# Performance work log

Hardware: AMD Instinct MI355X
Metric: run time of the kernel (lower is better)

## Reference

```python
import jax, jax.numpy as jnp
import numpy as np

HIDDEN = 128
GRID = 8
NEIGH = 4.0
CELL = NEIGH / GRID


def setup_inputs() -> dict:
    key = jax.random.key(0)
    k1, k2, k3, k4 = jax.random.split(key, 4)
    B, N = 64, 64
    hidden_states = jax.random.normal(k1, (B, N, HIDDEN), dtype=jnp.float32)
    positions = jax.random.normal(k2, (B, N, 2), dtype=jnp.float32)
    fan_in = HIDDEN * GRID * GRID
    bound = 1.0 / np.sqrt(fan_in)
    W = jax.random.uniform(k3, (HIDDEN, fan_in), minval=-bound, maxval=bound, dtype=jnp.float32)
    b = jax.random.uniform(k4, (HIDDEN,), minval=-bound, maxval=bound, dtype=jnp.float32)
    return {"hidden_states": hidden_states, "positions": positions, "W": W, "b": b}


def reference(hidden_states, positions, W, b):
    B, N, H = hidden_states.shape
    G, G2 = GRID, GRID * GRID
    # rel[b, i, j] = positions[b, j] - positions[b, i]  (offset of neighbor j in agent i's frame)
    rel = positions[:, None, :, :] - positions[:, :, None, :]  # [B, N, N, 2]
    # torch .long() truncates toward zero; jnp astype(int32) does the same, and after
    # clamping to [0, G-1] this matches the original exactly.
    gx = ((rel[..., 0] + NEIGH / 2) / CELL).astype(jnp.int32).clip(0, G - 1)
    gy = ((rel[..., 1] + NEIGH / 2) / CELL).astype(jnp.int32).clip(0, G - 1)
    cell = gx * G + gy  # [B, N(i), N(j)] flat grid-cell index (gx-major, matching view order)
    # Exclude self (j == i) from pooling.
    not_self = (1.0 - jnp.eye(N, dtype=hidden_states.dtype))  # [N(i), N(j)]
    onehot = jax.nn.one_hot(cell, G2, dtype=hidden_states.dtype) * not_self[None, :, :, None]
    # Scatter-add neighbor hidden states into each agent's grid: [B, N(i), G2, H]
    grid = jnp.einsum('bijc,bjh->bich', onehot, hidden_states)
    grid_flat = grid.reshape(B, N, G2 * H)  # (gx, gy, h) flatten order == torch .view
    pooled = grid_flat @ W.T + b  # [B, N, H]
    return pooled
```

## Files before the change

### kernel.cpp

```cpp
#include <hip/hip_runtime.h>
#include <hip/hip_bf16.h>
#include <stdint.h>


typedef __attribute__((ext_vector_type(8))) short bf16x8;
typedef __attribute__((ext_vector_type(4))) float f32x4;

#define NCHUNK 8
#define CPB 8

__device__ inline unsigned short bf16bits(float x) {
    __hip_bfloat16 h = __float2bfloat16(x);
    return *reinterpret_cast<unsigned short*>(&h);
}

__global__ __launch_bounds__(512)
void gp_wconv(const float* __restrict__ W, __hip_bfloat16* __restrict__ Wb)
{
    __shared__ __attribute__((aligned(16))) __hip_bfloat16 Wl[128][136];
    const int c = blockIdx.x, t = threadIdx.x;
    #pragma unroll
    for (int q = 0; q < 8; ++q) {
        int flat = q * 512 + t;
        int ho = flat >> 5, k4 = flat & 31;
        float4 v = *(const float4*)(W + (size_t)ho * 8192 + c * 128 + k4 * 4);
        __hip_bfloat16* d = &Wl[ho][k4 * 4];
        d[0] = __float2bfloat16(v.x); d[1] = __float2bfloat16(v.y);
        d[2] = __float2bfloat16(v.z); d[3] = __float2bfloat16(v.w);
    }
    __syncthreads();
    #pragma unroll
    for (int q = 0; q < 4; ++q) {
        int flat = q * 512 + t;
        int hg = flat >> 7, ho = flat & 127;
        bf16x8 v = *(const bf16x8*)&Wl[ho][hg * 8];
        *(bf16x8*)(Wb + (size_t)c * 16384 + (size_t)flat * 8) = v;
    }
}

__global__ __launch_bounds__(512, 4)
void gp_main(const float* __restrict__ hid, const float* __restrict__ pos,
             const __hip_bfloat16* __restrict__ Wb, float* __restrict__ partial)
{
    __shared__ __attribute__((aligned(16))) __hip_bfloat16 Hs[16 * 64 * 8];
    __shared__ __attribute__((aligned(16))) __hip_bfloat16 Zt[2][8 * 128 * 8];
    __shared__ __attribute__((aligned(16))) __hip_bfloat16 Ms[2][8 * 64 * 8];
    __shared__ unsigned char cellt[64 * 64];
    __shared__ float ps[128];

    const int t = threadIdx.x;
    const int b = blockIdx.x & 63, chunk = blockIdx.x >> 6;
    const int w = t >> 6, lane = t & 63;
    const int l15 = lane & 15, kg = lane >> 4;
    const int mw = w & 1, nw = w >> 1;

    if (t < 128) ps[t] = pos[(size_t)b * 128 + t];
    __syncthreads();

    #pragma unroll
    for (int q = 0; q < 8; ++q) {
        int idx = q * 512 + t;
        int i = idx >> 6, j = idx & 63;
        float rx = ps[j * 2 + 0] - ps[i * 2 + 0];
        float ry = ps[j * 2 + 1] - ps[i * 2 + 1];
        int gx = (int)((rx + 2.0f) * 2.0f);
        int gy = (int)((ry + 2.0f) * 2.0f);
        gx = gx < 0 ? 0 : (gx > 7 ? 7 : gx);
        gy = gy < 0 ? 0 : (gy > 7 ? 7 : gy);
        cellt[idx] = (i == j) ? 255 : (unsigned char)(gx * 8 + gy);
    }
    #pragma unroll
    for (int q = 0; q < 2; ++q) {
        int idx = q * 512 + t;
        int hg = idx >> 6, j = idx & 63;
        const float* src = hid + ((size_t)b * 64 + j) * 128 + hg * 8;
        float4 v0 = *(const float4*)src;
        float4 v1 = *(const float4*)(src + 4);
        __hip_bfloat16* d = &Hs[(hg * 64 + j) * 8];
        d[0] = __float2bfloat16(v0.x); d[1] = __float2bfloat16(v0.y);
        d[2] = __float2bfloat16(v0.z); d[3] = __float2bfloat16(v0.w);
        d[4] = __float2bfloat16(v1.x); d[5] = __float2bfloat16(v1.y);
        d[6] = __float2bfloat16(v1.z); d[7] = __float2bfloat16(v1.w);
    }
    __syncthreads();

    bf16x8 afr[2][4];
    #pragma unroll
    for (int ks = 0; ks < 4; ++ks) {
        int hg = ks * 4 + kg;
        afr[0][ks] = *(const bf16x8*)&Hs[(hg * 64 + mw * 32 + l15) * 8];
        afr[1][ks] = *(const bf16x8*)&Hs[(hg * 64 + mw * 32 + 16 + l15) * 8];
    }

    f32x4 acc[2][2];
    #pragma unroll
    for (int fm = 0; fm < 2; ++fm)
        #pragma unroll
        for (int fn = 0; fn < 2; ++fn)
            acc[fm][fn] = (f32x4){0.f, 0.f, 0.f, 0.f};

    #pragma unroll 2
    for (int cc = 0; cc < CPB; ++cc) {
        const int p = cc & 1;
        const int c = chunk * CPB + cc;

        const __hip_bfloat16* wc = Wb + (size_t)c * 16384;
        bf16x8 bfr[4][2];
        #pragma unroll
        for (int ks = 0; ks < 4; ++ks) {
            int hg = ks * 4 + kg;
            bfr[ks][0] = *(const bf16x8*)(wc + ((size_t)hg * 128 + nw * 32 + l15) * 8);
            bfr[ks][1] = *(const bf16x8*)(wc + ((size_t)hg * 128 + nw * 32 + 16 + l15) * 8);
        }

        {
            int i = t & 63, jg = t >> 6;
            const unsigned char* cr = &cellt[i * 64 + jg * 8];
            __hip_bfloat16* d = &Ms[p][(jg * 64 + i) * 8];
            #pragma unroll
            for (int e = 0; e < 8; ++e)
                d[e] = __float2bfloat16(cr[e] == c ? 1.0f : 0.0f);
        }

        f32x4 z[2][2];
        #pragma unroll
        for (int fm = 0; fm < 2; ++fm)
            #pragma unroll
            for (int fn = 0; fn < 2; ++fn)
                z[fm][fn] = (f32x4){0.f, 0.f, 0.f, 0.f};
        #pragma unroll
        for (int ks = 0; ks < 4; ++ks) {
            z[0][0] = __builtin_amdgcn_mfma_f32_16x16x32_bf16(afr[0][ks], bfr[ks][0], z[0][0], 0, 0, 0);
            z[0][1] = __builtin_amdgcn_mfma_f32_16x16x32_bf16(afr[0][ks], bfr[ks][1], z[0][1], 0, 0, 0);
            z[1][0] = __builtin_amdgcn_mfma_f32_16x16x32_bf16(afr[1][ks], bfr[ks][0], z[1][0], 0, 0, 0);
            z[1][1] = __builtin_amdgcn_mfma_f32_16x16x32_bf16(afr[1][ks], bfr[ks][1], z[1][1], 0, 0, 0);
        }

        #pragma unroll
        for (int fm = 0; fm < 2; ++fm) {
            #pragma unroll
            for (int fn = 0; fn < 2; ++fn) {
                int j0 = mw * 32 + fm * 16 + kg * 4;
                int jg = j0 >> 3, e0 = j0 & 7;
                int ho = nw * 32 + fn * 16 + l15;
                union { unsigned short us[4]; uint2 v; } pk;
                pk.us[0] = bf16bits(z[fm][fn][0]);
                pk.us[1] = bf16bits(z[fm][fn][1]);
                pk.us[2] = bf16bits(z[fm][fn][2]);
                pk.us[3] = bf16bits(z[fm][fn][3]);
                *(uint2*)((char*)&Zt[p][0] + ((size_t)(jg * 128 + ho) * 8 + e0) * 2) = pk.v;
            }
        }
        __syncthreads();

        #pragma unroll
        for (int ks = 0; ks < 2; ++ks) {
            int jg = ks * 4 + kg;
            bf16x8 a0 = *(const bf16x8*)&Ms[p][(jg * 64 + mw * 32 + l15) * 8];
            bf16x8 a1 = *(const bf16x8*)&Ms[p][(jg * 64 + mw * 32 + 16 + l15) * 8];
            bf16x8 b0 = *(const bf16x8*)&Zt[p][(jg * 128 + nw * 32 + l15) * 8];
            bf16x8 b1 = *(const bf16x8*)&Zt[p][(jg * 128 + nw * 32 + 16 + l15) * 8];
            acc[0][0] = __builtin_amdgcn_mfma_f32_16x16x32_bf16(a0, b0, acc[0][0], 0, 0, 0);
            acc[0][1] = __builtin_amdgcn_mfma_f32_16x16x32_bf16(a0, b1, acc[0][1], 0, 0, 0);
            acc[1][0] = __builtin_amdgcn_mfma_f32_16x16x32_bf16(a1, b0, acc[1][0], 0, 0, 0);
            acc[1][1] = __builtin_amdgcn_mfma_f32_16x16x32_bf16(a1, b1, acc[1][1], 0, 0, 0);
        }
    }

    float* pb = partial + (((size_t)chunk * 64 + b) * 64) * 128;
    #pragma unroll
    for (int fm = 0; fm < 2; ++fm)
        #pragma unroll
        for (int fn = 0; fn < 2; ++fn)
            #pragma unroll
            for (int r = 0; r < 4; ++r) {
                int i = mw * 32 + fm * 16 + kg * 4 + r;
                int ho = nw * 32 + fn * 16 + l15;
                pb[(size_t)i * 128 + ho] = acc[fm][fn][r];
            }
}

__global__ __launch_bounds__(512)
void gp_reduce(const float* __restrict__ partial, const float* __restrict__ bias,
               float* __restrict__ out)
{
    int gid = blockIdx.x * 512 + threadIdx.x;
    int ho4 = gid & 31;
    float4 a = *(const float4*)(bias + ho4 * 4);
    #pragma unroll
    for (int ch = 0; ch < NCHUNK; ++ch) {
        float4 v = *(const float4*)(partial + (size_t)ch * 524288 + (size_t)gid * 4);
        a.x += v.x; a.y += v.y; a.z += v.z; a.w += v.w;
    }
    *(float4*)(out + (size_t)gid * 4) = a;
}

extern "C" void kernel_launch(void* const* d_in, const int* in_sizes, int n_in,
                              void* d_out, int out_size, void* d_ws, size_t ws_size,
                              hipStream_t stream)
{
    const float* hid  = (const float*)d_in[0];
    const float* pos  = (const float*)d_in[1];
    const float* W    = (const float*)d_in[2];
    const float* bias = (const float*)d_in[3];
    float* out = (float*)d_out;

    __hip_bfloat16* Wb = (__hip_bfloat16*)d_ws;
    float* partial = (float*)((char*)d_ws + (size_t)2097152);

    hipLaunchKernelGGL(gp_wconv,  dim3(64),          dim3(512), 0, stream, W, Wb);
    hipLaunchKernelGGL(gp_main,   dim3(NCHUNK * 64), dim3(512), 0, stream, hid, pos, Wb, partial);
    hipLaunchKernelGGL(gp_reduce, dim3(256),         dim3(512), 0, stream, partial, bias, out);
}
```

Baseline: 34.25 us.

## Replace dense one-hot MFMA scatter with sparse per-cell neighbor lists

The second-stage dense MFMA against a mostly-zero one-hot mask is replaced. The kernel now builds per-agent, per-cell neighbor index lists in shared memory and sums the matching Z rows with scalar bf16-to-fp32 adds. Z is stored in an XOR-swizzled layout to reduce bank conflicts, and the accumulation for each cell is deferred one iteration so it overlaps the next cell's MFMA. W fragments are prefetched one cell ahead. The cost is data-dependent loop trip counts, which cause divergence and load imbalance across lanes, plus extra list-building passes over the cell table.

```diff
diff --git a/kernel.cpp b/kernel.cpp
--- a/kernel.cpp
+++ b/kernel.cpp
@@ -12,6 +12,11 @@
 __device__ inline unsigned short bf16bits(float x) {
     __hip_bfloat16 h = __float2bfloat16(x);
     return *reinterpret_cast<unsigned short*>(&h);
+}
+__device__ inline float bf2f(short u) {
+    union { unsigned int i; float f; } v;
+    v.i = ((unsigned int)(unsigned short)u) << 16;
+    return v.f;
 }
 
 __global__ __launch_bounds__(512)
@@ -43,16 +48,18 @@
              const __hip_bfloat16* __restrict__ Wb, float* __restrict__ partial)
 {
     __shared__ __attribute__((aligned(16))) __hip_bfloat16 Hs[16 * 64 * 8];
-    __shared__ __attribute__((aligned(16))) __hip_bfloat16 Zt[2][8 * 128 * 8];
-    __shared__ __attribute__((aligned(16))) __hip_bfloat16 Ms[2][8 * 64 * 8];
+    __shared__ __attribute__((aligned(16))) __hip_bfloat16 Zt[2][64 * 128];
     __shared__ unsigned char cellt[64 * 64];
+    __shared__ unsigned char listj[64 * 64];
+    __shared__ unsigned char cnt8[64][8];
+    __shared__ unsigned char offs[64][9];
     __shared__ float ps[128];
 
     const int t = threadIdx.x;
     const int b = blockIdx.x & 63, chunk = blockIdx.x >> 6;
     const int w = t >> 6, lane = t & 63;
     const int l15 = lane & 15, kg = lane >> 4;
-    const int mw = w & 1, nw = w >> 1;
+    const int wm = w & 3, wn = w >> 2;
 
     if (t < 128) ps[t] = pos[(size_t)b * 128 + t];
     __syncthreads();
@@ -84,100 +91,142 @@
     }
     __syncthreads();
 
-    bf16x8 afr[2][4];
+    bf16x8 hf[2][4];
     #pragma unroll
     for (int ks = 0; ks < 4; ++ks) {
         int hg = ks * 4 + kg;
-        afr[0][ks] = *(const bf16x8*)&Hs[(hg * 64 + mw * 32 + l15) * 8];
-        afr[1][ks] = *(const bf16x8*)&Hs[(hg * 64 + mw * 32 + 16 + l15) * 8];
-    }
-
-    f32x4 acc[2][2];
-    #pragma unroll
-    for (int fm = 0; fm < 2; ++fm)
-        #pragma unroll
-        for (int fn = 0; fn < 2; ++fn)
-            acc[fm][fn] = (f32x4){0.f, 0.f, 0.f, 0.f};
-
-    #pragma unroll 2
+        hf[0][ks] = *(const bf16x8*)&Hs[(hg * 64 + wn * 32 + l15) * 8];
+        hf[1][ks] = *(const bf16x8*)&Hs[(hg * 64 + wn * 32 + 16 + l15) * 8];
+    }
+
+    {
+        int i = t >> 3, c = t & 7;
+        int target = chunk * 8 + c;
+        int n = 0;
+        for (int j = 0; j < 64; ++j) n += (cellt[i * 64 + j] == target);
+        cnt8[i][c] = (unsigned char)n;
+    }
+    __syncthreads();
+    if (t < 64) {
+        int s = 0;
+        offs[t][0] = 0;
+        #pragma unroll
+        for (int c = 0; c < 8; ++c) { s += cnt8[t][c]; offs[t][c + 1] = (unsigned char)s; }
+    }
+    __syncthreads();
+    {
+        int i = t >> 3, c = t & 7;
+        int target = chunk * 8 + c;
+        int n = offs[i][c];
+        for (int j = 0; j < 64; ++j)
+            if (cellt[i * 64 + j] == target) listj[i * 64 + (n++)] = (unsigned char)j;
+    }
+
+    bf16x8 wf[2][4];
+    {
+        const __hip_bfloat16* wc = Wb + (size_t)(chunk * 8) * 16384;
+        #pragma unroll
+        for (int ks = 0; ks < 4; ++ks) {
+            int hg = ks * 4 + kg;
+            wf[0][ks] = *(const bf16x8*)(wc + ((size_t)hg * 128 + wm * 32 + l15) * 8);
+            wf[1][ks] = *(const bf16x8*)(wc + ((size_t)hg * 128 + wm * 32 + 16 + l15) * 8);
+        }
+    }
+
+    float acc[2][8];
+    #pragma unroll
+    for (int p4 = 0; p4 < 2; ++p4)
+        #pragma unroll
+        for (int e = 0; e < 8; ++e) acc[p4][e] = 0.f;
+
+    const int hog = lane & 15, ig = lane >> 4;
+    __syncthreads();
+
     for (int cc = 0; cc < CPB; ++cc) {
         const int p = cc & 1;
-        const int c = chunk * CPB + cc;
-
-        const __hip_bfloat16* wc = Wb + (size_t)c * 16384;
-        bf16x8 bfr[4][2];
+
+        if (cc > 0) {
+            const int cl = cc - 1;
+            #pragma unroll
+            for (int p4 = 0; p4 < 2; ++p4) {
+                int i = w * 8 + p4 * 4 + ig;
+                int n1 = offs[i][cl + 1];
+                for (int n = offs[i][cl]; n < n1; ++n) {
+                    int j = listj[i * 64 + n];
+                    int boff = (hog * 16) ^ ((j & 7) << 4);
+                    bf16x8 v = *(const bf16x8*)((const char*)&Zt[p ^ 1][0] + j * 256 + boff);
+                    #pragma unroll
+                    for (int e = 0; e < 8; ++e) acc[p4][e] += bf2f(v[e]);
+                }
+            }
+        }
+
+        f32x4 z[2][2];
+        #pragma unroll
+        for (int fm = 0; fm < 2; ++fm)
+            #pragma unroll
+            for (int fn = 0; fn < 2; ++fn) z[fm][fn] = (f32x4){0.f, 0.f, 0.f, 0.f};
         #pragma unroll
         for (int ks = 0; ks < 4; ++ks) {
-            int hg = ks * 4 + kg;
-            bfr[ks][0] = *(const bf16x8*)(wc + ((size_t)hg * 128 + nw * 32 + l15) * 8);
-            bfr[ks][1] = *(const bf16x8*)(wc + ((size_t)hg * 128 + nw * 32 + 16 + l15) * 8);
-        }
-
-        {
-            int i = t & 63, jg = t >> 6;
-            const unsigned char* cr = &cellt[i * 64 + jg * 8];
-            __hip_bfloat16* d = &Ms[p][(jg * 64 + i) * 8];
-            #pragma unroll
-            for (int e = 0; e < 8; ++e)
-                d[e] = __float2bfloat16(cr[e] == c ? 1.0f : 0.0f);
-        }
-
-        f32x4 z[2][2];
-        #pragma unroll
-        for (int fm = 0; fm < 2; ++fm)
-            #pragma unroll
-            for (int fn = 0; fn < 2; ++fn)
-                z[fm][fn] = (f32x4){0.f, 0.f, 0.f, 0.f};
-        #pragma unroll
-        for (int ks = 0; ks < 4; ++ks) {
-            z[0][0] = __builtin_amdgcn_mfma_f32_16x16x32_bf16(afr[0][ks], bfr[ks][0], z[0][0], 0, 0, 0);
-            z[0][1] = __builtin_amdgcn_mfma_f32_16x16x32_bf16(afr[0][ks], bfr[ks][1], z[0][1], 0, 0, 0);
-            z[1][0] = __builtin_amdgcn_mfma_f32_16x16x32_bf16(afr[1][ks], bfr[ks][0], z[1][0], 0, 0, 0);
-            z[1][1] = __builtin_amdgcn_mfma_f32_16x16x32_bf16(afr[1][ks], bfr[ks][1], z[1][1], 0, 0, 0);
+            z[0][0] = __builtin_amdgcn_mfma_f32_16x16x32_bf16(wf[0][ks], hf[0][ks], z[0][0], 0, 0, 0);
+            z[0][1] = __builtin_amdgcn_mfma_f32_16x16x32_bf16(wf[0][ks], hf[1][ks], z[0][1], 0, 0, 0);
+            z[1][0] = __builtin_amdgcn_mfma_f32_16x16x32_bf16(wf[1][ks], hf[0][ks], z[1][0], 0, 0, 0);
+            z[1][1] = __builtin_amdgcn_mfma_f32_16x16x32_bf16(wf[1][ks], hf[1][ks], z[1][1], 0, 0, 0);
         }
 
         #pragma unroll
         for (int fm = 0; fm < 2; ++fm) {
             #pragma unroll
             for (int fn = 0; fn < 2; ++fn) {
-                int j0 = mw * 32 + fm * 16 + kg * 4;
-                int jg = j0 >> 3, e0 = j0 & 7;
-                int ho = nw * 32 + fn * 16 + l15;
+                int j   = wn * 32 + fn * 16 + l15;
+                int ho0 = wm * 32 + fm * 16 + kg * 4;
+                int boff = (ho0 * 2) ^ ((j & 7) << 4);
                 union { unsigned short us[4]; uint2 v; } pk;
                 pk.us[0] = bf16bits(z[fm][fn][0]);
                 pk.us[1] = bf16bits(z[fm][fn][1]);
                 pk.us[2] = bf16bits(z[fm][fn][2]);
                 pk.us[3] = bf16bits(z[fm][fn][3]);
-                *(uint2*)((char*)&Zt[p][0] + ((size_t)(jg * 128 + ho) * 8 + e0) * 2) = pk.v;
+                *(uint2*)((char*)&Zt[p][0] + j * 256 + boff) = pk.v;
+            }
+        }
+
+        if (cc < CPB - 1) {
+            const __hip_bfloat16* wc = Wb + (size_t)(chunk * 8 + cc + 1) * 16384;
+            #pragma unroll
+            for (int ks = 0; ks < 4; ++ks) {
+                int hg = ks * 4 + kg;
+                wf[0][ks] = *(const bf16x8*)(wc + ((size_t)hg * 128 + wm * 32 + l15) * 8);
+                wf[1][ks] = *(const bf16x8*)(wc + ((size_t)hg * 128 + wm * 32 + 16 + l15) * 8);
             }
         }
         __syncthreads();
-
-        #pragma unroll
-        for (int ks = 0; ks < 2; ++ks) {
-            int jg = ks * 4 + kg;
-            bf16x8 a0 = *(const bf16x8*)&Ms[p][(jg * 64 + mw * 32 + l15) * 8];
-            bf16x8 a1 = *(const bf16x8*)&Ms[p][(jg * 64 + mw * 32 + 16 + l15) * 8];
-            bf16x8 b0 = *(const bf16x8*)&Zt[p][(jg * 128 + nw * 32 + l15) * 8];
-            bf16x8 b1 = *(const bf16x8*)&Zt[p][(jg * 128 + nw * 32 + 16 + l15) * 8];
-            acc[0][0] = __builtin_amdgcn_mfma_f32_16x16x32_bf16(a0, b0, acc[0][0], 0, 0, 0);
-            acc[0][1] = __builtin_amdgcn_mfma_f32_16x16x32_bf16(a0, b1, acc[0][1], 0, 0, 0);
-            acc[1][0] = __builtin_amdgcn_mfma_f32_16x16x32_bf16(a1, b0, acc[1][0], 0, 0, 0);
-            acc[1][1] = __builtin_amdgcn_mfma_f32_16x16x32_bf16(a1, b1, acc[1][1], 0, 0, 0);
+    }
+
+    {
+        const int cl = CPB - 1;
+        #pragma unroll
+        for (int p4 = 0; p4 < 2; ++p4) {
+            int i = w * 8 + p4 * 4 + ig;
+            int n1 = offs[i][cl + 1];
+            for (int n = offs[i][cl]; n < n1; ++n) {
+                int j = listj[i * 64 + n];
+                int boff = (hog * 16) ^ ((j & 7) << 4);
+                bf16x8 v = *(const bf16x8*)((const char*)&Zt[(CPB - 1) & 1][0] + j * 256 + boff);
+                #pragma unroll
+                for (int e = 0; e < 8; ++e) acc[p4][e] += bf2f(v[e]);
+            }
         }
     }
 
     float* pb = partial + (((size_t)chunk * 64 + b) * 64) * 128;
     #pragma unroll
-    for (int fm = 0; fm < 2; ++fm)
-        #pragma unroll
-        for (int fn = 0; fn < 2; ++fn)
-            #pragma unroll
-            for (int r = 0; r < 4; ++r) {
-                int i = mw * 32 + fm * 16 + kg * 4 + r;
-                int ho = nw * 32 + fn * 16 + l15;
-                pb[(size_t)i * 128 + ho] = acc[fm][fn][r];
-            }
+    for (int p4 = 0; p4 < 2; ++p4) {
+        int i = w * 8 + p4 * 4 + ig;
+        float4 v0 = make_float4(acc[p4][0], acc[p4][1], acc[p4][2], acc[p4][3]);
+        float4 v1 = make_float4(acc[p4][4], acc[p4][5], acc[p4][6], acc[p4][7]);
+        *(float4*)(pb + (size_t)i * 128 + hog * 8) = v0;
+        *(float4*)(pb + (size_t)i * 128 + hog * 8 + 4) = v1;
+    }
 }
 
 __global__ __launch_bounds__(512)
```

After: 47.71 us. 39.3% more time.

## Double-buffer W chunks in LDS via async global_load_lds prefetch

Applied to the files above, without the earlier changes.

Each per-cell W tile is no longer loaded from global memory into registers per wave. The block now copies it into a double-buffered LDS array with global_load_lds, prefetching the next cell's tile while the current one is computed, and the MFMA B-fragments are read from LDS. This aims to hide global load latency and remove the duplicate W loads across waves. In exchange, LDS use grows by 64KB and the occupancy hint drops from 4 to 2, which cuts resident blocks per CU. It also relies on the barrier correctly waiting for the asynchronous LDS loads.

```diff
diff --git a/kernel.cpp b/kernel.cpp
--- a/kernel.cpp
+++ b/kernel.cpp
@@ -8,6 +8,12 @@
 
 #define NCHUNK 8
 #define CPB 8
+
+__device__ inline void load_lds16(const void* g, void* l) {
+    __builtin_amdgcn_global_load_lds(
+        (const __attribute__((address_space(1))) unsigned int*)g,
+        (__attribute__((address_space(3))) unsigned int*)l, 16, 0, 0);
+}
 
 __device__ inline unsigned short bf16bits(float x) {
     __hip_bfloat16 h = __float2bfloat16(x);
@@ -38,10 +44,11 @@
     }
 }
 
-__global__ __launch_bounds__(512, 4)
+__global__ __launch_bounds__(512, 2)
 void gp_main(const float* __restrict__ hid, const float* __restrict__ pos,
              const __hip_bfloat16* __restrict__ Wb, float* __restrict__ partial)
 {
+    __shared__ __attribute__((aligned(16))) __hip_bfloat16 Ws[2][16 * 128 * 8];
     __shared__ __attribute__((aligned(16))) __hip_bfloat16 Hs[16 * 64 * 8];
     __shared__ __attribute__((aligned(16))) __hip_bfloat16 Zt[2][8 * 128 * 8];
     __shared__ __attribute__((aligned(16))) __hip_bfloat16 Ms[2][8 * 64 * 8];
@@ -82,6 +89,15 @@
         d[4] = __float2bfloat16(v1.x); d[5] = __float2bfloat16(v1.y);
         d[6] = __float2bfloat16(v1.z); d[7] = __float2bfloat16(v1.w);
     }
+
+    {
+        const char* gsrc = (const char*)(Wb + (size_t)(chunk * 8) * 16384);
+        #pragma unroll
+        for (int q = 0; q < 4; ++q) {
+            int off = q * 8192 + t * 16;
+            load_lds16(gsrc + off, (char*)&Ws[0][0] + off);
+        }
+    }
     __syncthreads();
 
     bf16x8 afr[2][4];
@@ -104,13 +120,13 @@
         const int p = cc & 1;
         const int c = chunk * CPB + cc;
 
-        const __hip_bfloat16* wc = Wb + (size_t)c * 16384;
-        bf16x8 bfr[4][2];
-        #pragma unroll
-        for (int ks = 0; ks < 4; ++ks) {
-            int hg = ks * 4 + kg;
-            bfr[ks][0] = *(const bf16x8*)(wc + ((size_t)hg * 128 + nw * 32 + l15) * 8);
-            bfr[ks][1] = *(const bf16x8*)(wc + ((size_t)hg * 128 + nw * 32 + 16 + l15) * 8);
+        if (cc < CPB - 1) {
+            const char* gsrc = (const char*)(Wb + (size_t)(c + 1) * 16384);
+            #pragma unroll
+            for (int q = 0; q < 4; ++q) {
+                int off = q * 8192 + t * 16;
+                load_lds16(gsrc + off, (char*)&Ws[p ^ 1][0] + off);
+            }
         }
 
         {
@@ -126,14 +142,16 @@
         #pragma unroll
         for (int fm = 0; fm < 2; ++fm)
             #pragma unroll
-            for (int fn = 0; fn < 2; ++fn)
-                z[fm][fn] = (f32x4){0.f, 0.f, 0.f, 0.f};
+            for (int fn = 0; fn < 2; ++fn) z[fm][fn] = (f32x4){0.f, 0.f, 0.f, 0.f};
         #pragma unroll
         for (int ks = 0; ks < 4; ++ks) {
-            z[0][0] = __builtin_amdgcn_mfma_f32_16x16x32_bf16(afr[0][ks], bfr[ks][0], z[0][0], 0, 0, 0);
-            z[0][1] = __builtin_amdgcn_mfma_f32_16x16x32_bf16(afr[0][ks], bfr[ks][1], z[0][1], 0, 0, 0);
-            z[1][0] = __builtin_amdgcn_mfma_f32_16x16x32_bf16(afr[1][ks], bfr[ks][0], z[1][0], 0, 0, 0);
-            z[1][1] = __builtin_amdgcn_mfma_f32_16x16x32_bf16(afr[1][ks], bfr[ks][1], z[1][1], 0, 0, 0);
+            int hg = ks * 4 + kg;
+            bf16x8 b0 = *(const bf16x8*)&Ws[p][(hg * 128 + nw * 32 + l15) * 8];
+            bf16x8 b1 = *(const bf16x8*)&Ws[p][(hg * 128 + nw * 32 + 16 + l15) * 8];
+            z[0][0] = __builtin_amdgcn_mfma_f32_16x16x32_bf16(afr[0][ks], b0, z[0][0], 0, 0, 0);
+            z[0][1] = __builtin_amdgcn_mfma_f32_16x16x32_bf16(afr[0][ks], b1, z[0][1], 0, 0, 0);
+            z[1][0] = __builtin_amdgcn_mfma_f32_16x16x32_bf16(afr[1][ks], b0, z[1][0], 0, 0, 0);
+            z[1][1] = __builtin_amdgcn_mfma_f32_16x16x32_bf16(afr[1][ks], b1, z[1][1], 0, 0, 0);
         }
 
         #pragma unroll
```

Measured after the change: 37.93 us. +10.7%, slower.

## Restructure gp_main into per-wave independent pipelines without block barriers

Applied to the files above, without the earlier changes.

Halves the block to 256 threads, with each wave owning a 32-column output slice and all 64 rows. Each wave now computes its own Z tile into a private swizzled LDS scratch and reads it back, so the per-cell __syncthreads is gone. The one-hot mask is built in registers from preloaded cell bytes instead of staged through LDS. W fragments for the next cell are double-buffered in registers. The cost is higher register pressure (a 4x4 array of A fragments, 8 accumulators and two W buffers) and fewer waves per block, which may reduce occupancy.

```diff
diff --git a/kernel.cpp b/kernel.cpp
--- a/kernel.cpp
+++ b/kernel.cpp
@@ -5,6 +5,7 @@
 
 typedef __attribute__((ext_vector_type(8))) short bf16x8;
 typedef __attribute__((ext_vector_type(4))) float f32x4;
+typedef unsigned int u32;
 
 #define NCHUNK 8
 #define CPB 8
@@ -38,13 +39,12 @@
     }
 }
 
-__global__ __launch_bounds__(512, 4)
+__global__ __launch_bounds__(256, 2)
 void gp_main(const float* __restrict__ hid, const float* __restrict__ pos,
              const __hip_bfloat16* __restrict__ Wb, float* __restrict__ partial)
 {
     __shared__ __attribute__((aligned(16))) __hip_bfloat16 Hs[16 * 64 * 8];
-    __shared__ __attribute__((aligned(16))) __hip_bfloat16 Zt[2][8 * 128 * 8];
-    __shared__ __attribute__((aligned(16))) __hip_bfloat16 Ms[2][8 * 64 * 8];
+    __shared__ u32 zscr[4][1024];
     __shared__ unsigned char cellt[64 * 64];
     __shared__ float ps[128];
 
@@ -52,14 +52,13 @@
     const int b = blockIdx.x & 63, chunk = blockIdx.x >> 6;
     const int w = t >> 6, lane = t & 63;
     const int l15 = lane & 15, kg = lane >> 4;
-    const int mw = w & 1, nw = w >> 1;
 
     if (t < 128) ps[t] = pos[(size_t)b * 128 + t];
     __syncthreads();
 
     #pragma unroll
-    for (int q = 0; q < 8; ++q) {
-        int idx = q * 512 + t;
+    for (int q = 0; q < 16; ++q) {
+        int idx = q * 256 + t;
         int i = idx >> 6, j = idx & 63;
         float rx = ps[j * 2 + 0] - ps[i * 2 + 0];
         float ry = ps[j * 2 + 1] - ps[i * 2 + 1];
@@ -70,8 +69,8 @@
         cellt[idx] = (i == j) ? 255 : (unsigned char)(gx * 8 + gy);
     }
     #pragma unroll
-    for (int q = 0; q < 2; ++q) {
-        int idx = q * 512 + t;
+    for (int q = 0; q < 4; ++q) {
+        int idx = q * 256 + t;
         int hg = idx >> 6, j = idx & 63;
         const float* src = hid + ((size_t)b * 64 + j) * 128 + hg * 8;
         float4 v0 = *(const float4*)src;
@@ -84,99 +83,125 @@
     }
     __syncthreads();
 
-    bf16x8 afr[2][4];
-    #pragma unroll
-    for (int ks = 0; ks < 4; ++ks) {
-        int hg = ks * 4 + kg;
-        afr[0][ks] = *(const bf16x8*)&Hs[(hg * 64 + mw * 32 + l15) * 8];
-        afr[1][ks] = *(const bf16x8*)&Hs[(hg * 64 + mw * 32 + 16 + l15) * 8];
-    }
-
-    f32x4 acc[2][2];
-    #pragma unroll
-    for (int fm = 0; fm < 2; ++fm)
-        #pragma unroll
-        for (int fn = 0; fn < 2; ++fn)
-            acc[fm][fn] = (f32x4){0.f, 0.f, 0.f, 0.f};
-
-    #pragma unroll 2
+    bf16x8 a[4][4];
+    #pragma unroll
+    for (int jt = 0; jt < 4; ++jt)
+        #pragma unroll
+        for (int ks = 0; ks < 4; ++ks) {
+            int hg = ks * 4 + kg;
+            a[jt][ks] = *(const bf16x8*)&Hs[(hg * 64 + jt * 16 + l15) * 8];
+        }
+    uint2 cs[4][2];
+    #pragma unroll
+    for (int mt = 0; mt < 4; ++mt)
+        #pragma unroll
+        for (int ks2 = 0; ks2 < 2; ++ks2)
+            cs[mt][ks2] = *(const uint2*)&cellt[(mt * 16 + l15) * 64 + ks2 * 32 + kg * 8];
+
+    f32x4 acc[4][2];
+    #pragma unroll
+    for (int mt = 0; mt < 4; ++mt) {
+        acc[mt][0] = (f32x4){0.f, 0.f, 0.f, 0.f};
+        acc[mt][1] = (f32x4){0.f, 0.f, 0.f, 0.f};
+    }
+
+    u32* zw = &zscr[w][0];
+
+    bf16x8 wf[2][4][2];
+    {
+        const __hip_bfloat16* wc = Wb + (size_t)(chunk * CPB) * 16384;
+        #pragma unroll
+        for (int ks = 0; ks < 4; ++ks)
+            #pragma unroll
+            for (int fh = 0; fh < 2; ++fh)
+                wf[0][ks][fh] = *(const bf16x8*)(wc +
+                    ((size_t)(ks * 4 + kg) * 128 + w * 32 + fh * 16 + l15) * 8);
+    }
+
+    #pragma unroll
     for (int cc = 0; cc < CPB; ++cc) {
         const int p = cc & 1;
         const int c = chunk * CPB + cc;
 
-        const __hip_bfloat16* wc = Wb + (size_t)c * 16384;
-        bf16x8 bfr[4][2];
-        #pragma unroll
-        for (int ks = 0; ks < 4; ++ks) {
-            int hg = ks * 4 + kg;
-            bfr[ks][0] = *(const bf16x8*)(wc + ((size_t)hg * 128 + nw * 32 + l15) * 8);
-            bfr[ks][1] = *(const bf16x8*)(wc + ((size_t)hg * 128 + nw * 32 + 16 + l15) * 8);
-        }
-
-        {
-            int i = t & 63, jg = t >> 6;
-            const unsigned char* cr = &cellt[i * 64 + jg * 8];
-            __hip_bfloat16* d = &Ms[p][(jg * 64 + i) * 8];
-            #pragma unroll
-            for (int e = 0; e < 8; ++e)
-                d[e] = __float2bfloat16(cr[e] == c ? 1.0f : 0.0f);
-        }
-
-        f32x4 z[2][2];
-        #pragma unroll
-        for (int fm = 0; fm < 2; ++fm)
-            #pragma unroll
-            for (int fn = 0; fn < 2; ++fn)
-                z[fm][fn] = (f32x4){0.f, 0.f, 0.f, 0.f};
-        #pragma unroll
-        for (int ks = 0; ks < 4; ++ks) {
-            z[0][0] = __builtin_amdgcn_mfma_f32_16x16x32_bf16(afr[0][ks], bfr[ks][0], z[0][0], 0, 0, 0);
-            z[0][1] = __builtin_amdgcn_mfma_f32_16x16x32_bf16(afr[0][ks], bfr[ks][1], z[0][1], 0, 0, 0);
-            z[1][0] = __builtin_amdgcn_mfma_f32_16x16x32_bf16(afr[1][ks], bfr[ks][0], z[1][0], 0, 0, 0);
-            z[1][1] = __builtin_amdgcn_mfma_f32_16x16x32_bf16(afr[1][ks], bfr[ks][1], z[1][1], 0, 0, 0);
-        }
-
-        #pragma unroll
-        for (int fm = 0; fm < 2; ++fm) {
-            #pragma unroll
-            for (int fn = 0; fn < 2; ++fn) {
-                int j0 = mw * 32 + fm * 16 + kg * 4;
-                int jg = j0 >> 3, e0 = j0 & 7;
-                int ho = nw * 32 + fn * 16 + l15;
-                union { unsigned short us[4]; uint2 v; } pk;
-                pk.us[0] = bf16bits(z[fm][fn][0]);
-                pk.us[1] = bf16bits(z[fm][fn][1]);
-                pk.us[2] = bf16bits(z[fm][fn][2]);
-                pk.us[3] = bf16bits(z[fm][fn][3]);
-                *(uint2*)((char*)&Zt[p][0] + ((size_t)(jg * 128 + ho) * 8 + e0) * 2) = pk.v;
-            }
-        }
-        __syncthreads();
-
-        #pragma unroll
-        for (int ks = 0; ks < 2; ++ks) {
-            int jg = ks * 4 + kg;
-            bf16x8 a0 = *(const bf16x8*)&Ms[p][(jg * 64 + mw * 32 + l15) * 8];
-            bf16x8 a1 = *(const bf16x8*)&Ms[p][(jg * 64 + mw * 32 + 16 + l15) * 8];
-            bf16x8 b0 = *(const bf16x8*)&Zt[p][(jg * 128 + nw * 32 + l15) * 8];
-            bf16x8 b1 = *(const bf16x8*)&Zt[p][(jg * 128 + nw * 32 + 16 + l15) * 8];
-            acc[0][0] = __builtin_amdgcn_mfma_f32_16x16x32_bf16(a0, b0, acc[0][0], 0, 0, 0);
-            acc[0][1] = __builtin_amdgcn_mfma_f32_16x16x32_bf16(a0, b1, acc[0][1], 0, 0, 0);
-            acc[1][0] = __builtin_amdgcn_mfma_f32_16x16x32_bf16(a1, b0, acc[1][0], 0, 0, 0);
-            acc[1][1] = __builtin_amdgcn_mfma_f32_16x16x32_bf16(a1, b1, acc[1][1], 0, 0, 0);
+        if (cc + 1 < CPB) {
+            const __hip_bfloat16* wc = Wb + (size_t)(c + 1) * 16384;
+            #pragma unroll
+            for (int ks = 0; ks < 4; ++ks)
+                #pragma unroll
+                for (int fh = 0; fh < 2; ++fh)
+                    wf[p ^ 1][ks][fh] = *(const bf16x8*)(wc +
+                        ((size_t)(ks * 4 + kg) * 128 + w * 32 + fh * 16 + l15) * 8);
+        }
+
+        f32x4 z[4][2];
+        #pragma unroll
+        for (int jt = 0; jt < 4; ++jt) {
+            z[jt][0] = (f32x4){0.f, 0.f, 0.f, 0.f};
+            z[jt][1] = (f32x4){0.f, 0.f, 0.f, 0.f};
+        }
+        #pragma unroll
+        for (int ks = 0; ks < 4; ++ks)
+            #pragma unroll
+            for (int jt = 0; jt < 4; ++jt) {
+                z[jt][0] = __builtin_amdgcn_mfma_f32_16x16x32_bf16(a[jt][ks], wf[p][ks][0], z[jt][0], 0, 0, 0);
+                z[jt][1] = __builtin_amdgcn_mfma_f32_16x16x32_bf16(a[jt][ks], wf[p][ks][1], z[jt][1], 0, 0, 0);
+            }
+
+        #pragma unroll
+        for (int jt = 0; jt < 4; ++jt)
+            #pragma unroll
+            for (int fh = 0; fh < 2; ++fh) {
+                u32 p0 = (u32)bf16bits(z[jt][fh][0]) | ((u32)bf16bits(z[jt][fh][1]) << 16);
+                u32 p1 = (u32)bf16bits(z[jt][fh][2]) | ((u32)bf16bits(z[jt][fh][3]) << 16);
+                int X = ((jt * 2 + (kg >> 1)) & 3) << 3;
+                int a32 = (((jt * 8 + kg * 2) * 32) + fh * 16 + l15) ^ X;
+                zw[a32] = p0;
+                zw[a32 + 32] = p1;
+            }
+
+        bf16x8 b2[2][2];
+        #pragma unroll
+        for (int ks2 = 0; ks2 < 2; ++ks2)
+            #pragma unroll
+            for (int fh = 0; fh < 2; ++fh) {
+                int base = (((ks2 * 16 + kg * 4) * 32) + fh * 16 + l15) ^ (kg << 3);
+                union { u32 wd[4]; bf16x8 v; } r;
+                r.wd[0] = zw[base];
+                r.wd[1] = zw[base + 32];
+                r.wd[2] = zw[base + 64];
+                r.wd[3] = zw[base + 96];
+                b2[ks2][fh] = r.v;
+            }
+
+        #pragma unroll
+        for (int mt = 0; mt < 4; ++mt) {
+            #pragma unroll
+            for (int ks2 = 0; ks2 < 2; ++ks2) {
+                union { u32 wd[4]; bf16x8 v; } m;
+                u32 s0 = cs[mt][ks2].x, s1 = cs[mt][ks2].y;
+                #pragma unroll
+                for (int k = 0; k < 4; ++k) {
+                    u32 s = (k < 2) ? s0 : s1;
+                    u32 b0 = (s >> ((k & 1) * 16)) & 0xFFu;
+                    u32 b1 = (s >> ((k & 1) * 16 + 8)) & 0xFFu;
+                    m.wd[k] = (b0 == (u32)c ? 0x3F80u : 0u) | (b1 == (u32)c ? 0x3F800000u : 0u);
+                }
+                acc[mt][0] = __builtin_amdgcn_mfma_f32_16x16x32_bf16(m.v, b2[ks2][0], acc[mt][0], 0, 0, 0);
+                acc[mt][1] = __builtin_amdgcn_mfma_f32_16x16x32_bf16(m.v, b2[ks2][1], acc[mt][1], 0, 0, 0);
+            }
         }
     }
 
     float* pb = partial + (((size_t)chunk * 64 + b) * 64) * 128;
     #pragma unroll
-    for (int fm = 0; fm < 2; ++fm)
-        #pragma unroll
-        for (int fn = 0; fn < 2; ++fn)
+    for (int mt = 0; mt < 4; ++mt)
+        #pragma unroll
+        for (int fh = 0; fh < 2; ++fh)
             #pragma unroll
             for (int r = 0; r < 4; ++r) {
-                int i = mw * 32 + fm * 16 + kg * 4 + r;
-                int ho = nw * 32 + fn * 16 + l15;
-                pb[(size_t)i * 128 + ho] = acc[fm][fn][r];
+                int i = mt * 16 + kg * 4 + r;
+                int ho = w * 32 + fh * 16 + l15;
+                pb[(size_t)i * 128 + ho] = acc[mt][fh][r];
             }
 }
 
@@ -209,6 +234,6 @@
     float* partial = (float*)((char*)d_ws + (size_t)2097152);
 
     hipLaunchKernelGGL(gp_wconv,  dim3(64),          dim3(512), 0, stream, W, Wb);
-    hipLaunchKernelGGL(gp_main,   dim3(NCHUNK * 64), dim3(512), 0, stream, hid, pos, Wb, partial);
+    hipLaunchKernelGGL(gp_main,   dim3(NCHUNK * 64), dim3(256), 0, stream, hid, pos, Wb, partial);
     hipLaunchKernelGGL(gp_reduce, dim3(256),         dim3(512), 0, stream, partial, bias, out);
 }
```

Measured after the change: 38.42 us. +12.2%, slower.
